# Kernel tuning notes

Hardware: AMD Instinct MI355X
Metric: run time of the kernel (lower is better)

## Reference

```python
import jax, jax.numpy as jnp
import numpy as np

OUT = 7   # roi_output_size
SR = 2    # fixed sampling ratio (torchvision default -1 is adaptive per-box; fixed 2 is the standard jit-friendly choice)


def _bilinear(fm, y, x):
    # fm [C,H,W]; y,x [P] -> [C,P], torchvision roi_align boundary rules
    C, H, W = fm.shape
    valid = (y >= -1.0) & (y <= H) & (x >= -1.0) & (x <= W)
    y = jnp.clip(y, 0.0, H - 1.0)
    x = jnp.clip(x, 0.0, W - 1.0)
    y0 = jnp.floor(y).astype(jnp.int32)
    x0 = jnp.floor(x).astype(jnp.int32)
    y1 = jnp.minimum(y0 + 1, H - 1)
    x1 = jnp.minimum(x0 + 1, W - 1)
    ly = y - y0
    lx = x - x0
    hy = 1.0 - ly
    hx = 1.0 - lx
    v = (fm[:, y0, x0] * (hy * hx) + fm[:, y0, x1] * (hy * lx)
         + fm[:, y1, x0] * (ly * hx) + fm[:, y1, x1] * (ly * lx))
    return jnp.where(valid, v, 0.0)


def _roi_align_one(fm, bx):
    # fm [C,H,W], bx [N,4] (x1,y1,x2,y2) -> [N, C*OUT*OUT]; aligned=True, spatial_scale=1.0
    N = bx.shape[0]
    C = fm.shape[0]
    x1 = bx[:, 0] - 0.5
    y1 = bx[:, 1] - 0.5
    x2 = bx[:, 2] - 0.5
    y2 = bx[:, 3] - 0.5
    bin_h = (y2 - y1) / OUT
    bin_w = (x2 - x1) / OUT
    grid = jnp.arange(OUT)[:, None] + (jnp.arange(SR) + 0.5)[None, :] / SR   # [OUT,SR]
    ys = y1[:, None, None] + grid[None] * bin_h[:, None, None]              # [N,OUT,SR]
    xs = x1[:, None, None] + grid[None] * bin_w[:, None, None]
    Y = jnp.broadcast_to(ys[:, :, :, None, None], (N, OUT, SR, OUT, SR)).reshape(-1)
    X = jnp.broadcast_to(xs[:, None, None, :, :], (N, OUT, SR, OUT, SR)).reshape(-1)
    v = _bilinear(fm, Y, X).reshape(C, N, OUT, SR, OUT, SR)
    pooled = v.mean(axis=(3, 5))                # [C,N,OUT,OUT] average over samples in each bin
    return pooled.transpose(1, 0, 2, 3).reshape(N, -1)  # [N, C*49], matches torch flatten(1)


def _forward(feat, boxes, w_roi, b_roi, sev_query, w_in, b_in, w_out, b_out, ln_g, ln_b, w1, b1, w2, b2):
    B = feat.shape[0]
    hidden = w_roi.shape[0]
    nh = 4
    hd = hidden // nh
    pooled = jax.vmap(_roi_align_one)(feat, boxes)          # [B,N,C*49]
    tokens = pooled @ w_roi.T + b_roi                       # [B,N,hidden]
    q = jnp.broadcast_to(sev_query, (B, 1, hidden))
    wq, wk, wv = w_in[:hidden], w_in[hidden:2 * hidden], w_in[2 * hidden:]
    bq, bk, bv = b_in[:hidden], b_in[hidden:2 * hidden], b_in[2 * hidden:]
    qh = (q @ wq.T + bq).reshape(B, 1, nh, hd).transpose(0, 2, 1, 3)        # [B,h,1,d]
    kh = (tokens @ wk.T + bk).reshape(B, -1, nh, hd).transpose(0, 2, 1, 3)  # [B,h,N,d]
    vh = (tokens @ wv.T + bv).reshape(B, -1, nh, hd).transpose(0, 2, 1, 3)
    scores = jnp.einsum('bhqd,bhkd->bhqk', qh, kh) / jnp.sqrt(jnp.float32(hd))
    att = jax.nn.softmax(scores, axis=-1)
    ctx = jnp.einsum('bhqk,bhkd->bhqd', att, vh).transpose(0, 2, 1, 3).reshape(B, 1, hidden)
    o = (ctx @ w_out.T + b_out)[:, 0]                       # [B,hidden]
    mu = o.mean(-1, keepdims=True)
    var = o.var(-1, keepdims=True)
    x = (o - mu) / jnp.sqrt(var + 1e-5) * ln_g + ln_b       # LayerNorm
    h = jax.nn.relu(x @ w1.T + b1)                          # dropout is identity in eval
    return h @ w2.T + b2                                    # [B,num_classes]


def setup_inputs() -> dict:
    k = jax.random.split(jax.random.key(0), 8)
    B, C, H, W = 16, 256, 200, 200
    N, hidden, num_classes = 100, 256, 4
    roi_dim = C * OUT * OUT
    s = 0.02
    feat = jax.random.normal(k[0], (B, C, H, W), jnp.float32)
    u = jax.random.uniform(k[1], (B, N, 4), jnp.float32)
    x1 = u[..., 0] * (W - 70.0)
    y1 = u[..., 1] * (H - 70.0)
    boxes = jnp.stack([x1, y1, x1 + 6.0 + u[..., 2] * 60.0, y1 + 6.0 + u[..., 3] * 60.0], axis=-1)
    return dict(
        feat=feat, boxes=boxes,
        w_roi=jax.random.normal(k[2], (hidden, roi_dim), jnp.float32) * s,
        b_roi=jnp.zeros((hidden,), jnp.float32),
        sev_query=jax.random.normal(k[3], (1, 1, hidden), jnp.float32) * s,
        w_in=jax.random.normal(k[4], (3 * hidden, hidden), jnp.float32) * s,
        b_in=jnp.zeros((3 * hidden,), jnp.float32),
        w_out=jax.random.normal(k[5], (hidden, hidden), jnp.float32) * s,
        b_out=jnp.zeros((hidden,), jnp.float32),
        ln_g=jnp.ones((hidden,), jnp.float32),
        ln_b=jnp.zeros((hidden,), jnp.float32),
        w1=jax.random.normal(k[6], (hidden, hidden), jnp.float32) * s,
        b1=jnp.zeros((hidden,), jnp.float32),
        w2=jax.random.normal(k[7], (num_classes, hidden), jnp.float32) * s,
        b2=jnp.zeros((num_classes,), jnp.float32),
    )


def reference(feat, boxes, w_roi, b_roi, sev_query, w_in, b_in, w_out, b_out, ln_g, ln_b, w1, b1, w2, b2):
    return _forward(feat, boxes, w_roi, b_roi, sev_query, w_in, b_in, w_out, b_out, ln_g, ln_b, w1, b1, w2, b2)
```

## Files before the change

### kernel.cpp

```cpp
#include <hip/hip_runtime.h>
#include <math.h>

#define B_    16
#define C_    256
#define H_    200
#define W_    200
#define NBOX  100
#define HID   256
#define OUTK  7
#define ROI_DIM 12544
#define KP    25088
#define NCLS  4

struct __attribute__((packed, aligned(4))) f2u { float x, y; };

typedef __attribute__((ext_vector_type(8))) short short8v;
typedef __attribute__((ext_vector_type(4))) float f32x4;

static __device__ __forceinline__ unsigned short f2bf(float f) {
  unsigned u = __float_as_uint(f);
  return (unsigned short)((u + 0x7FFFu + ((u >> 16) & 1u)) >> 16);
}
static __device__ __forceinline__ float bf2f(unsigned short h) {
  return __uint_as_float(((unsigned)h) << 16);
}

__global__ __launch_bounds__(256) void boxtab_kernel(
    const float* __restrict__ boxes, int2* __restrict__ ytab, int2* __restrict__ xtab)
{
  int t = blockIdx.x * 256 + threadIdx.x;
  if (t >= B_ * NBOX * 14) return;
  int s14 = t % 14;
  int ib  = t / 14;
  const float* bx = boxes + (size_t)ib * 4;
  int i = s14 >> 1, s = s14 & 1;
  float fo = (float)i + 0.25f + 0.5f * (float)s;
  {
    float y1 = bx[1] - 0.5f;
    float bh = (bx[3] - 0.5f - y1) * (1.0f / 7.0f);
    float yc = fminf(fmaxf(y1 + fo * bh, 0.0f), 199.0f);
    int y0 = min((int)yc, 198);
    ytab[(size_t)ib * 14 + s14] = make_int2(y0 * W_, __float_as_int(yc - (float)y0));
  }
  {
    float x1 = bx[0] - 0.5f;
    float bw = (bx[2] - 0.5f - x1) * (1.0f / 7.0f);
    float xc = fminf(fmaxf(x1 + fo * bw, 0.0f), 199.0f);
    int x0 = min((int)xc, 198);
    xtab[(size_t)ib * 14 + s14] = make_int2(x0, __float_as_int(xc - (float)x0));
  }
}

__global__ __launch_bounds__(1024, 8) void roi_pool_kernel(
    const float* __restrict__ feat, const int2* __restrict__ ytab,
    const int2* __restrict__ xtab, unsigned* __restrict__ Ap32)
{
  extern __shared__ unsigned short lmap[];
  int bid = blockIdx.x;
  int img = bid >> 8;
  int ch  = bid & 255;
  int tid = threadIdx.x;

  const float4* src = (const float4*)(feat + ((size_t)img * C_ + ch) * (H_ * W_));
  #pragma unroll
  for (int r = 0; r < 9; ++r) {
    int i = tid + r * 1024;
    float4 v = src[i];
    ushort4 h = make_ushort4(f2bf(v.x), f2bf(v.y), f2bf(v.z), f2bf(v.w));
    *(ushort4*)(lmap + i * 4) = h;
  }
  {
    int i = tid + 9 * 1024;
    if (i < 10000) {
      float4 v = src[i];
      ushort4 h = make_ushort4(f2bf(v.x), f2bf(v.y), f2bf(v.z), f2bf(v.w));
      *(ushort4*)(lmap + i * 4) = h;
    }
  }
  __syncthreads();

  const int4* yt = (const int4*)(ytab + (size_t)img * NBOX * 14);
  const int4* xt = (const int4*)(xtab + (size_t)img * NBOX * 14);
  unsigned* ap = Ap32 + (size_t)img * NBOX * ROI_DIM + ch * 49;

  #pragma unroll
  for (int rnd = 0; rnd < 5; ++rnd) {
    int it = tid + rnd * 1024;
    if (it < NBOX * 49) {
      int box = it / 49;
      int bin = it - box * 49;
      int bi  = bin / 7;
      int bj  = bin - bi * 7;

      int4 yw = yt[box * 7 + bi];
      int4 xw = xt[box * 7 + bj];
      int   yr0 = yw.x, yr1 = yw.z;
      float ly0 = __int_as_float(yw.y), ly1 = __int_as_float(yw.w);
      int   xc0 = xw.x, xc1 = xw.z;
      float lx0 = __int_as_float(xw.y), lx1 = __int_as_float(xw.w);
      float hy0 = 1.0f - ly0, hy1 = 1.0f - ly1;
      float hx0 = 1.0f - lx0, hx1 = 1.0f - lx1;

      int p00 = yr0 + xc0, p01 = yr0 + xc1;
      int p10 = yr0 + W_ + xc0, p11 = yr0 + W_ + xc1;
      int q00 = yr1 + xc0, q01 = yr1 + xc1;
      int q10 = yr1 + W_ + xc0, q11 = yr1 + W_ + xc1;

      float sum =
          hy0 * (hx0 * bf2f(lmap[p00]) + lx0 * bf2f(lmap[p00 + 1]))
        + ly0 * (hx0 * bf2f(lmap[p10]) + lx0 * bf2f(lmap[p10 + 1]))
        + hy0 * (hx1 * bf2f(lmap[p01]) + lx1 * bf2f(lmap[p01 + 1]))
        + ly0 * (hx1 * bf2f(lmap[p11]) + lx1 * bf2f(lmap[p11 + 1]))
        + hy1 * (hx0 * bf2f(lmap[q00]) + lx0 * bf2f(lmap[q00 + 1]))
        + ly1 * (hx0 * bf2f(lmap[q10]) + lx0 * bf2f(lmap[q10 + 1]))
        + hy1 * (hx1 * bf2f(lmap[q01]) + lx1 * bf2f(lmap[q01 + 1]))
        + ly1 * (hx1 * bf2f(lmap[q11]) + lx1 * bf2f(lmap[q11 + 1]));

      float s = sum * 0.25f;
      unsigned short hi = f2bf(s);
      unsigned short lo = f2bf(s - bf2f(hi));
      ap[(size_t)box * ROI_DIM + bin] = (unsigned)hi | ((unsigned)lo << 16);
    }
  }
}

__global__ __launch_bounds__(256) void wconv_kernel(
    const float* __restrict__ w, unsigned* __restrict__ Bp32)
{
  int i = blockIdx.x * 256 + threadIdx.x;
  unsigned short hi = f2bf(w[i]);
  Bp32[i] = (unsigned)hi | ((unsigned)hi << 16);
}

#define GBM 64
#define GBN 256
#define GBK 64
#define KSP 14
#define KT  28
__global__ __launch_bounds__(256) void gemm_kernel(
    const unsigned short* __restrict__ Ap,
    const unsigned short* __restrict__ Bp,
    float* __restrict__ Cpart)
{
  __shared__ __align__(16) short As[GBM * GBK];
  __shared__ __align__(16) short Bs[GBN * GBK];

  int tid  = threadIdx.x;
  int lane = tid & 63;
  int w    = tid >> 6;
  int wr   = w >> 1, wc = w & 1;
  int m0 = blockIdx.x * GBM;
  int z  = blockIdx.y;
  int kbase = z * (GBK * KT);

  f32x4 acc[2][8];
  #pragma unroll
  for (int mi = 0; mi < 2; ++mi)
    #pragma unroll
    for (int nj = 0; nj < 8; ++nj)
      acc[mi][nj] = (f32x4){0.f, 0.f, 0.f, 0.f};

  for (int kt = 0; kt < KT; ++kt) {
    int kg = kbase + kt * GBK;
    __syncthreads();
    #pragma unroll
    for (int r = 0; r < 2; ++r) {
      int q = tid + r * 256;
      int row = q >> 3, c16 = q & 7;
      int kc16 = c16 ^ (row & 7);
      short8v v = *(const short8v*)(Ap + (size_t)(m0 + row) * KP + kg + kc16 * 8);
      *(short8v*)(As + row * GBK + c16 * 8) = v;
    }
    #pragma unroll
    for (int r = 0; r < 8; ++r) {
      int q = tid + r * 256;
      int row = q >> 3, c16 = q & 7;
      int kc16 = c16 ^ (row & 7);
      short8v v = *(const short8v*)(Bp + (size_t)row * KP + kg + kc16 * 8);
      *(short8v*)(Bs + row * GBK + c16 * 8) = v;
    }
    __syncthreads();
    #pragma unroll
    for (int kk = 0; kk < 2; ++kk) {
      short8v af[2], bf[8];
      #pragma unroll
      for (int mi = 0; mi < 2; ++mi) {
        int row = wr * 32 + mi * 16 + (lane & 15);
        int c16 = (kk * 4 + (lane >> 4)) ^ (row & 7);
        af[mi] = *(const short8v*)(As + row * GBK + c16 * 8);
      }
      #pragma unroll
      for (int nj = 0; nj < 8; ++nj) {
        int row = wc * 128 + nj * 16 + (lane & 15);
        int c16 = (kk * 4 + (lane >> 4)) ^ (row & 7);
        bf[nj] = *(const short8v*)(Bs + row * GBK + c16 * 8);
      }
      #pragma unroll
      for (int mi = 0; mi < 2; ++mi)
        #pragma unroll
        for (int nj = 0; nj < 8; ++nj)
          acc[mi][nj] = __builtin_amdgcn_mfma_f32_16x16x32_bf16(
              af[mi], bf[nj], acc[mi][nj], 0, 0, 0);
    }
  }
  float* part = Cpart + (size_t)z * (B_ * NBOX * HID);
  int cn = lane & 15, rg = lane >> 4;
  #pragma unroll
  for (int mi = 0; mi < 2; ++mi)
    #pragma unroll
    for (int nj = 0; nj < 8; ++nj)
      #pragma unroll
      for (int r = 0; r < 4; ++r) {
        int row = m0 + wr * 32 + mi * 16 + rg * 4 + r;
        int col = wc * 128 + nj * 16 + cn;
        part[(size_t)row * HID + col] = acc[mi][nj][r];
      }
}

__global__ __launch_bounds__(256) void reduce_kernel(
    const float* __restrict__ Cpart, const float* __restrict__ b_roi,
    float* __restrict__ tokens)
{
  int i = blockIdx.x * 256 + threadIdx.x;
  const float4* bias4 = (const float4*)b_roi;
  float4 a = bias4[i & 63];
  const float4* cp = (const float4*)Cpart;
  #pragma unroll
  for (int z = 0; z < KSP; ++z) {
    float4 p = cp[(size_t)z * (B_ * NBOX * HID / 4) + i];
    a.x += p.x; a.y += p.y; a.z += p.z; a.w += p.w;
  }
  ((float4*)tokens)[i] = a;
}

__global__ __launch_bounds__(256) void attn_kernel(
    const float* __restrict__ tokens, const float* __restrict__ sev_q,
    const float* __restrict__ w_in,  const float* __restrict__ b_in,
    float* __restrict__ ctx)
{
  __shared__ float qh_s[64], qkv_s[256], att_s[128], tbar_s[256], red_s[2];
  int bh = blockIdx.x;
  int b = bh >> 2, h = bh & 3;
  int tid = threadIdx.x;
  const float* tok = tokens + (size_t)b * NBOX * HID;

  if (tid < 64) {
    const float* wq = w_in + (size_t)(h * 64 + tid) * HID;
    float a = 0.0f;
    for (int e = 0; e < HID; ++e) a += sev_q[e] * wq[e];
    qh_s[tid] = a + b_in[h * 64 + tid];
  }
  __syncthreads();
  {
    float a = 0.0f;
    for (int d = 0; d < 64; ++d)
      a += qh_s[d] * w_in[(size_t)(256 + h * 64 + d) * HID + tid];
    qkv_s[tid] = a;
  }
  if (tid == 0) {
    float a = 0.0f;
    for (int d = 0; d < 64; ++d) a += qh_s[d] * b_in[256 + h * 64 + d];
    red_s[0] = a;
  }
  __syncthreads();
  if (tid < NBOX) {
    const float4* tr = (const float4*)(tok + (size_t)tid * HID);
    const float4* qv = (const float4*)qkv_s;
    float a = 0.0f;
    for (int e = 0; e < 64; ++e) {
      float4 t4 = tr[e], q4 = qv[e];
      a += t4.x * q4.x + t4.y * q4.y + t4.z * q4.z + t4.w * q4.w;
    }
    att_s[tid] = (a + red_s[0]) * 0.125f;
  }
  __syncthreads();
  if (tid == 0) {
    float mx = -1e30f;
    for (int t = 0; t < NBOX; ++t) mx = fmaxf(mx, att_s[t]);
    float sm = 0.0f;
    for (int t = 0; t < NBOX; ++t) { float e = expf(att_s[t] - mx); att_s[t] = e; sm += e; }
    red_s[1] = 1.0f / sm;
  }
  __syncthreads();
  {
    float a = 0.0f;
    for (int t = 0; t < NBOX; ++t) a += att_s[t] * tok[(size_t)t * HID + tid];
    tbar_s[tid] = a * red_s[1];
  }
  __syncthreads();
  if (tid < 64) {
    const float* wv = w_in + (size_t)(512 + h * 64 + tid) * HID;
    float a = 0.0f;
    for (int e = 0; e < HID; ++e) a += tbar_s[e] * wv[e];
    ctx[(size_t)b * HID + h * 64 + tid] = a + b_in[512 + h * 64 + tid];
  }
}

__global__ __launch_bounds__(256) void mlp_kernel(
    const float* __restrict__ ctx,
    const float* __restrict__ w_out, const float* __restrict__ b_out,
    const float* __restrict__ ln_g,  const float* __restrict__ ln_b,
    const float* __restrict__ w1,    const float* __restrict__ b1,
    const float* __restrict__ w2,    const float* __restrict__ b2,
    float* __restrict__ outp)
{
  __shared__ float o_s[256], x_s[256], h1_s[256], red_s[8];
  int b = blockIdx.x, tid = threadIdx.x;
  const float* cx = ctx + (size_t)b * HID;
  {
    const float* wo = w_out + (size_t)tid * HID;
    float a = 0.0f;
    for (int k = 0; k < HID; ++k) a += cx[k] * wo[k];
    o_s[tid] = a + b_out[tid];
  }
  __syncthreads();
  {
    float v = o_s[tid];
    float s1 = v, s2 = v * v;
    #pragma unroll
    for (int off = 32; off > 0; off >>= 1) {
      s1 += __shfl_down(s1, off);
      s2 += __shfl_down(s2, off);
    }
    if ((tid & 63) == 0) { red_s[(tid >> 6) * 2] = s1; red_s[(tid >> 6) * 2 + 1] = s2; }
    __syncthreads();
    float sum = red_s[0] + red_s[2] + red_s[4] + red_s[6];
    float ssq = red_s[1] + red_s[3] + red_s[5] + red_s[7];
    float mu  = sum * (1.0f / 256.0f);
    float var = ssq * (1.0f / 256.0f) - mu * mu;
    float inv = rsqrtf(var + 1e-5f);
    x_s[tid] = (v - mu) * inv * ln_g[tid] + ln_b[tid];
  }
  __syncthreads();
  {
    const float* wr = w1 + (size_t)tid * HID;
    float a = 0.0f;
    for (int k = 0; k < HID; ++k) a += x_s[k] * wr[k];
    h1_s[tid] = fmaxf(a + b1[tid], 0.0f);
  }
  __syncthreads();
  if (tid < NCLS) {
    const float* wr = w2 + (size_t)tid * HID;
    float a = 0.0f;
    for (int k = 0; k < HID; ++k) a += h1_s[k] * wr[k];
    outp[b * NCLS + tid] = a + b2[tid];
  }
}

extern "C" void kernel_launch(void* const* d_in, const int* in_sizes, int n_in,
                              void* d_out, int out_size, void* d_ws, size_t ws_size,
                              hipStream_t stream) {
  (void)in_sizes; (void)n_in; (void)out_size; (void)ws_size;
  const float* feat  = (const float*)d_in[0];
  const float* boxes = (const float*)d_in[1];
  const float* w_roi = (const float*)d_in[2];
  const float* b_roi = (const float*)d_in[3];
  const float* sev_q = (const float*)d_in[4];
  const float* w_in  = (const float*)d_in[5];
  const float* b_in  = (const float*)d_in[6];
  const float* w_out = (const float*)d_in[7];
  const float* b_out = (const float*)d_in[8];
  const float* ln_g  = (const float*)d_in[9];
  const float* ln_b  = (const float*)d_in[10];
  const float* w1    = (const float*)d_in[11];
  const float* b1    = (const float*)d_in[12];
  const float* w2    = (const float*)d_in[13];
  const float* b2    = (const float*)d_in[14];
  float* out = (float*)d_out;

  unsigned short* Ap = (unsigned short*)d_ws;
  unsigned short* Bp = Ap + (size_t)B_ * NBOX * KP;
  float* Cpart  = (float*)(Bp + (size_t)HID * KP);
  float* tokens = Cpart + (size_t)KSP * B_ * NBOX * HID;
  float* ctx    = tokens + (size_t)B_ * NBOX * HID;
  int2* ytab    = (int2*)(ctx + B_ * HID);
  int2* xtab    = ytab + (size_t)B_ * NBOX * 14;

  boxtab_kernel  <<<(B_ * NBOX * 14 + 255) / 256, 256, 0, stream>>>(boxes, ytab, xtab);
  roi_pool_kernel<<<B_ * C_, 1024, 80000, stream>>>(feat, ytab, xtab, (unsigned*)Ap);
  wconv_kernel   <<<(HID * ROI_DIM) / 256, 256, 0, stream>>>(w_roi, (unsigned*)Bp);
  gemm_kernel    <<<dim3((B_ * NBOX) / GBM, KSP), 256, 0, stream>>>(Ap, Bp, Cpart);
  reduce_kernel  <<<(B_ * NBOX * HID / 4) / 256, 256, 0, stream>>>(Cpart, b_roi, tokens);
  attn_kernel    <<<B_ * 4, 256, 0, stream>>>(tokens, sev_q, w_in, b_in, ctx);
  mlp_kernel     <<<B_, 256, 0, stream>>>(ctx, w_out, b_out, ln_g, ln_b,
                                          w1, b1, w2, b2, out);
}
```

Baseline: 276.6 us.

## Double-buffer feature-map channels in ROI pooling with register prefetch

Each ROI pooling block now handles 16 channels of one image instead of a single channel, using two LDS buffers. The next channel's feature map is loaded into registers while the current channel is sampled, then converted to bf16 and written to the other buffer, so global loads overlap with the bilinear gather. This needs 160 KB of shared memory per block and ten float4 prefetch registers per thread. The grid shrinks to 256 blocks, roughly one per CU, which costs parallelism and latency hiding from multiple resident blocks.

```diff
diff --git a/kernel.cpp b/kernel.cpp
--- a/kernel.cpp
+++ b/kernel.cpp
@@ -24,6 +24,9 @@
 static __device__ __forceinline__ float bf2f(unsigned short h) {
   return __uint_as_float(((unsigned)h) << 16);
 }
+static __device__ __forceinline__ ushort4 cvt4(float4 v) {
+  return make_ushort4(f2bf(v.x), f2bf(v.y), f2bf(v.z), f2bf(v.w));
+}
 
 __global__ __launch_bounds__(256) void boxtab_kernel(
     const float* __restrict__ boxes, int2* __restrict__ ytab, int2* __restrict__ xtab)
@@ -51,76 +54,108 @@
   }
 }
 
-__global__ __launch_bounds__(1024, 8) void roi_pool_kernel(
+__global__ __launch_bounds__(1024, 4) void roi_pool_kernel(
     const float* __restrict__ feat, const int2* __restrict__ ytab,
     const int2* __restrict__ xtab, unsigned* __restrict__ Ap32)
 {
-  extern __shared__ unsigned short lmap[];
+  extern __shared__ unsigned short smem[];
+  unsigned short* buf0 = smem;
+  unsigned short* buf1 = smem + 40000;
+
   int bid = blockIdx.x;
-  int img = bid >> 8;
-  int ch  = bid & 255;
+  int img = bid >> 4;
+  int ch0 = (bid & 15) * 16;
   int tid = threadIdx.x;
-
-  const float4* src = (const float4*)(feat + ((size_t)img * C_ + ch) * (H_ * W_));
-  #pragma unroll
-  for (int r = 0; r < 9; ++r) {
-    int i = tid + r * 1024;
-    float4 v = src[i];
-    ushort4 h = make_ushort4(f2bf(v.x), f2bf(v.y), f2bf(v.z), f2bf(v.w));
-    *(ushort4*)(lmap + i * 4) = h;
-  }
-  {
-    int i = tid + 9 * 1024;
-    if (i < 10000) {
-      float4 v = src[i];
-      ushort4 h = make_ushort4(f2bf(v.x), f2bf(v.y), f2bf(v.z), f2bf(v.w));
-      *(ushort4*)(lmap + i * 4) = h;
-    }
-  }
-  __syncthreads();
 
   const int4* yt = (const int4*)(ytab + (size_t)img * NBOX * 14);
   const int4* xt = (const int4*)(xtab + (size_t)img * NBOX * 14);
-  unsigned* ap = Ap32 + (size_t)img * NBOX * ROI_DIM + ch * 49;
-
-  #pragma unroll
-  for (int rnd = 0; rnd < 5; ++rnd) {
-    int it = tid + rnd * 1024;
-    if (it < NBOX * 49) {
-      int box = it / 49;
-      int bin = it - box * 49;
-      int bi  = bin / 7;
-      int bj  = bin - bi * 7;
-
-      int4 yw = yt[box * 7 + bi];
-      int4 xw = xt[box * 7 + bj];
-      int   yr0 = yw.x, yr1 = yw.z;
-      float ly0 = __int_as_float(yw.y), ly1 = __int_as_float(yw.w);
-      int   xc0 = xw.x, xc1 = xw.z;
-      float lx0 = __int_as_float(xw.y), lx1 = __int_as_float(xw.w);
-      float hy0 = 1.0f - ly0, hy1 = 1.0f - ly1;
-      float hx0 = 1.0f - lx0, hx1 = 1.0f - lx1;
-
-      int p00 = yr0 + xc0, p01 = yr0 + xc1;
-      int p10 = yr0 + W_ + xc0, p11 = yr0 + W_ + xc1;
-      int q00 = yr1 + xc0, q01 = yr1 + xc1;
-      int q10 = yr1 + W_ + xc0, q11 = yr1 + W_ + xc1;
-
-      float sum =
-          hy0 * (hx0 * bf2f(lmap[p00]) + lx0 * bf2f(lmap[p00 + 1]))
-        + ly0 * (hx0 * bf2f(lmap[p10]) + lx0 * bf2f(lmap[p10 + 1]))
-        + hy0 * (hx1 * bf2f(lmap[p01]) + lx1 * bf2f(lmap[p01 + 1]))
-        + ly0 * (hx1 * bf2f(lmap[p11]) + lx1 * bf2f(lmap[p11 + 1]))
-        + hy1 * (hx0 * bf2f(lmap[q00]) + lx0 * bf2f(lmap[q00 + 1]))
-        + ly1 * (hx0 * bf2f(lmap[q10]) + lx0 * bf2f(lmap[q10 + 1]))
-        + hy1 * (hx1 * bf2f(lmap[q01]) + lx1 * bf2f(lmap[q01 + 1]))
-        + ly1 * (hx1 * bf2f(lmap[q11]) + lx1 * bf2f(lmap[q11 + 1]));
-
-      float s = sum * 0.25f;
-      unsigned short hi = f2bf(s);
-      unsigned short lo = f2bf(s - bf2f(hi));
-      ap[(size_t)box * ROI_DIM + bin] = (unsigned)hi | ((unsigned)lo << 16);
-    }
+  unsigned* apb = Ap32 + (size_t)img * NBOX * ROI_DIM;
+
+  const float4* fbase = (const float4*)(feat + ((size_t)img * C_ + ch0) * (H_ * W_));
+
+  {
+    #pragma unroll
+    for (int r = 0; r < 9; ++r) {
+      int i = tid + r * 1024;
+      *(ushort4*)(buf0 + i * 4) = cvt4(fbase[i]);
+    }
+    int i = tid + 9 * 1024;
+    if (i < 10000) *(ushort4*)(buf0 + i * 4) = cvt4(fbase[i]);
+  }
+  __syncthreads();
+
+  #pragma unroll 1
+  for (int n = 0; n < 16; ++n) {
+    const unsigned short* cur = (n & 1) ? buf1 : buf0;
+    unsigned short*       nxt = (n & 1) ? buf0 : buf1;
+
+    float4 rv0, rv1, rv2, rv3, rv4, rv5, rv6, rv7, rv8, rv9;
+    if (n < 15) {
+      const float4* src = fbase + (size_t)(n + 1) * (H_ * W_ / 4);
+      rv0 = src[tid];            rv1 = src[tid + 1024];
+      rv2 = src[tid + 2048];     rv3 = src[tid + 3072];
+      rv4 = src[tid + 4096];     rv5 = src[tid + 5120];
+      rv6 = src[tid + 6144];     rv7 = src[tid + 7168];
+      rv8 = src[tid + 8192];
+      if (tid < 784) rv9 = src[tid + 9216];
+    }
+    __builtin_amdgcn_sched_barrier(0);
+
+    unsigned* ap = apb + (size_t)(ch0 + n) * 49;
+    #pragma unroll
+    for (int rnd = 0; rnd < 5; ++rnd) {
+      int it = tid + rnd * 1024;
+      if (it < NBOX * 49) {
+        int box = it / 49;
+        int bin = it - box * 49;
+        int bi  = bin / 7;
+        int bj  = bin - bi * 7;
+
+        int4 yw = yt[box * 7 + bi];
+        int4 xw = xt[box * 7 + bj];
+        int   yr0 = yw.x, yr1 = yw.z;
+        float ly0 = __int_as_float(yw.y), ly1 = __int_as_float(yw.w);
+        int   xc0 = xw.x, xc1 = xw.z;
+        float lx0 = __int_as_float(xw.y), lx1 = __int_as_float(xw.w);
+        float hy0 = 1.0f - ly0, hy1 = 1.0f - ly1;
+        float hx0 = 1.0f - lx0, hx1 = 1.0f - lx1;
+
+        int p00 = yr0 + xc0, p01 = yr0 + xc1;
+        int p10 = yr0 + W_ + xc0, p11 = yr0 + W_ + xc1;
+        int q00 = yr1 + xc0, q01 = yr1 + xc1;
+        int q10 = yr1 + W_ + xc0, q11 = yr1 + W_ + xc1;
+
+        float sum =
+            hy0 * (hx0 * bf2f(cur[p00]) + lx0 * bf2f(cur[p00 + 1]))
+          + ly0 * (hx0 * bf2f(cur[p10]) + lx0 * bf2f(cur[p10 + 1]))
+          + hy0 * (hx1 * bf2f(cur[p01]) + lx1 * bf2f(cur[p01 + 1]))
+          + ly0 * (hx1 * bf2f(cur[p11]) + lx1 * bf2f(cur[p11 + 1]))
+          + hy1 * (hx0 * bf2f(cur[q00]) + lx0 * bf2f(cur[q00 + 1]))
+          + ly1 * (hx0 * bf2f(cur[q10]) + lx0 * bf2f(cur[q10 + 1]))
+          + hy1 * (hx1 * bf2f(cur[q01]) + lx1 * bf2f(cur[q01 + 1]))
+          + ly1 * (hx1 * bf2f(cur[q11]) + lx1 * bf2f(cur[q11 + 1]));
+
+        float s = sum * 0.25f;
+        unsigned short hi = f2bf(s);
+        unsigned short lo = f2bf(s - bf2f(hi));
+        ap[(size_t)box * ROI_DIM + bin] = (unsigned)hi | ((unsigned)lo << 16);
+      }
+    }
+    __builtin_amdgcn_sched_barrier(0);
+
+    if (n < 15) {
+      *(ushort4*)(nxt + (tid         ) * 4) = cvt4(rv0);
+      *(ushort4*)(nxt + (tid +  1024) * 4) = cvt4(rv1);
+      *(ushort4*)(nxt + (tid +  2048) * 4) = cvt4(rv2);
+      *(ushort4*)(nxt + (tid +  3072) * 4) = cvt4(rv3);
+      *(ushort4*)(nxt + (tid +  4096) * 4) = cvt4(rv4);
+      *(ushort4*)(nxt + (tid +  5120) * 4) = cvt4(rv5);
+      *(ushort4*)(nxt + (tid +  6144) * 4) = cvt4(rv6);
+      *(ushort4*)(nxt + (tid +  7168) * 4) = cvt4(rv7);
+      *(ushort4*)(nxt + (tid +  8192) * 4) = cvt4(rv8);
+      if (tid < 784) *(ushort4*)(nxt + (tid + 9216) * 4) = cvt4(rv9);
+    }
+    __syncthreads();
   }
 }
 
@@ -377,7 +412,7 @@
   int2* xtab    = ytab + (size_t)B_ * NBOX * 14;
 
   boxtab_kernel  <<<(B_ * NBOX * 14 + 255) / 256, 256, 0, stream>>>(boxes, ytab, xtab);
-  roi_pool_kernel<<<B_ * C_, 1024, 80000, stream>>>(feat, ytab, xtab, (unsigned*)Ap);
+  roi_pool_kernel<<<B_ * 16, 1024, 160000, stream>>>(feat, ytab, xtab, (unsigned*)Ap);
   wconv_kernel   <<<(HID * ROI_DIM) / 256, 256, 0, stream>>>(w_roi, (unsigned*)Bp);
   gemm_kernel    <<<dim3((B_ * NBOX) / GBM, KSP), 256, 0, stream>>>(Ap, Bp, Cpart);
   reduce_kernel  <<<(B_ * NBOX * HID / 4) / 256, 256, 0, stream>>>(Cpart, b_roi, tokens);
```

Result: slower. 306.6 us (+10.8%).
